# Performance work log

Hardware: AMD Instinct MI355X
Metric: run time of the kernel (lower is better)

Reference implementation:

```python
import jax, jax.numpy as jnp
import numpy as np

HEADS = 8
NEG_SLOPE = 0.2


def _layer_norm(x, g, b, eps=1e-5):
    mu = x.mean(-1, keepdims=True)
    var = ((x - mu) ** 2).mean(-1, keepdims=True)
    return (x - mu) / jnp.sqrt(var + eps) * g + b


def setup_inputs() -> dict:
    key = jax.random.key(0)
    ks = jax.random.split(key, 24)
    N, E, H, L = 512, 260000, 256, 4
    s = 0.05
    return dict(
        x=jax.random.normal(ks[0], (N, 1), jnp.float32),
        edge_index=jax.random.randint(ks[1], (2, E), 0, N),
        edge_attr=jax.random.uniform(ks[2], (E, 3), jnp.float32),
        emb_W=jax.random.normal(ks[3], (1, H)) * s,
        emb_b=jnp.zeros((H,)),
        Wl=jax.random.normal(ks[4], (L, H, H)) * s,
        bl=jnp.zeros((L, H)),
        Wr=jax.random.normal(ks[5], (L, H, H)) * s,
        br=jnp.zeros((L, H)),
        We=jax.random.normal(ks[6], (L, 3, H)) * s,
        att=jax.random.normal(ks[7], (L, HEADS, H // HEADS)) * s,
        gb=jnp.zeros((L, H)),
        ln_g=jnp.ones((L, H)),
        ln_b=jnp.zeros((L, H)),
        p1_W=jax.random.normal(ks[8], (2 * H, H)) * s,
        p1_b=jnp.zeros((H,)),
        p2_W=jax.random.normal(ks[9], (H, H // 2)) * s,
        p2_b=jnp.zeros((H // 2,)),
        p3_W=jax.random.normal(ks[10], (H // 2, 1)) * s,
        p3_b=jnp.zeros((1,)),
        v1_W=jax.random.normal(ks[11], (2 * H, H)) * s,
        v1_b=jnp.zeros((H,)),
        v2_W=jax.random.normal(ks[12], (H, 1)) * s,
        v2_b=jnp.zeros((1,)),
        coupling=jnp.asarray(1.0, jnp.float32),
    )


def reference(x, edge_index, edge_attr, emb_W, emb_b, Wl, bl, Wr, br, We, att,
              gb, ln_g, ln_b, p1_W, p1_b, p2_W, p2_b, p3_W, p3_b,
              v1_W, v1_b, v2_W, v2_b, coupling):
    N = x.shape[0]
    E = edge_attr.shape[0]
    L = Wl.shape[0]
    C = Wl.shape[-1] // HEADS
    src, dst = edge_index[0], edge_index[1]

    # PyG GATv2Conv adds self-loops with edge_attr fill_value='mean'
    # (mean of incoming edge_attr per destination node).
    sums = jax.ops.segment_sum(edge_attr, dst, num_segments=N)
    cnt = jax.ops.segment_sum(jnp.ones((E,), edge_attr.dtype), dst, num_segments=N)
    self_attr = sums / jnp.maximum(cnt, 1.0)[:, None]
    loop = jnp.arange(N)
    src_f = jnp.concatenate([src, loop])            # [E+N]
    dst_f = jnp.concatenate([dst, loop])
    ea_f = jnp.concatenate([edge_attr, self_attr])  # [E+N, 3]

    h = x @ emb_W + emb_b                           # [N, H]
    for l in range(L):
        res = h
        xl = (h @ Wl[l] + bl[l]).reshape(N, HEADS, C)
        xr = (h @ Wr[l] + br[l]).reshape(N, HEADS, C)
        ee = (ea_f @ We[l]).reshape(-1, HEADS, C)
        # GATv2 scoring: leaky_relu(x_l[src]+x_r[dst]+edge) . att
        m = jax.nn.leaky_relu(xl[src_f] + xr[dst_f] + ee, NEG_SLOPE)
        alpha = jnp.einsum('ehc,hc->eh', m, att[l])
        amax = jax.ops.segment_max(alpha, dst_f, num_segments=N)
        alpha = jnp.exp(alpha - amax[dst_f])
        denom = jax.ops.segment_sum(alpha, dst_f, num_segments=N)
        alpha = alpha / denom[dst_f]
        out = jax.ops.segment_sum(xl[src_f] * alpha[..., None], dst_f,
                                  num_segments=N).reshape(N, HEADS * C) + gb[l]
        h = jax.nn.relu(_layer_norm(out + res, ln_g[l], ln_b[l]))

    # graph-level representation (single graph, batch=None branch)
    graph_repr = jnp.concatenate([h.mean(0, keepdims=True),
                                  h.max(0, keepdims=True)], axis=1)  # [1, 2H]

    # all-pairs edge representations (i < j)
    iu, ju = jnp.triu_indices(N, k=1)
    er = jnp.concatenate([h[iu], h[ju]], axis=1)    # [N(N-1)/2, 2H]
    p = jax.nn.relu(er @ p1_W + p1_b)
    p = jax.nn.relu(p @ p2_W + p2_b)
    policy_logits = (p @ p3_W + p3_b).squeeze(-1)   # [N(N-1)/2]

    v = jax.nn.relu(graph_repr @ v1_W + v1_b)
    value = (v @ v2_W + v2_b).squeeze(-1)           # [1]

    # Potts energy: per-color degree-squared approximation of triangles
    colors = jnp.argmax(edge_attr, axis=1)
    energy = jnp.asarray(0.0, h.dtype)
    for c in (1, 2):
        w = (colors == c).astype(h.dtype)
        deg = (jax.ops.segment_sum(w, src, num_segments=N)
               + jax.ops.segment_sum(w, dst, num_segments=N))
        energy = energy + (deg ** 2).sum() / (2.0 * N)
    energy = energy * coupling

    return policy_logits, value, energy
```

## Files before the change

### kernel.cpp

```cpp
#include <hip/hip_runtime.h>
#include <math.h>

#define HDIM 256
#define NHEADS 8
#define NEG 0.2f
#define NB 256
#define SEG 4

typedef float f32x4 __attribute__((ext_vector_type(4)));
typedef _Float16 f16x8 __attribute__((ext_vector_type(8)));
typedef __fp16 fp16v2 __attribute__((ext_vector_type(2)));

__global__ __launch_bounds__(256) void edge_part(
    const int* __restrict__ ei, const float* __restrict__ ea, int E, int CH,
    int* __restrict__ pcnt, float* __restrict__ psum, int* __restrict__ pcol) {
  __shared__ int   lcnt[512];
  __shared__ float ls0[512], ls1[512], ls2[512];
  __shared__ int   lcol[1024];
  int t = threadIdx.x, b = blockIdx.x;
  for (int n = t; n < 512; n += 256) {
    lcnt[n] = 0; ls0[n] = 0.f; ls1[n] = 0.f; ls2[n] = 0.f;
    lcol[n] = 0; lcol[512 + n] = 0;
  }
  __syncthreads();
  int e0 = b * CH, e1 = min(E, e0 + CH);
  for (int e = e0 + t; e < e1; e += 256) {
    int src = ei[e], dst = ei[E + e];
    float a0 = ea[3*e], a1 = ea[3*e+1], a2 = ea[3*e+2];
    atomicAdd(&lcnt[dst], 1);
    atomicAdd(&ls0[dst], a0);
    atomicAdd(&ls1[dst], a1);
    atomicAdd(&ls2[dst], a2);
    int idx = 0; float best = a0;
    if (a1 > best) { best = a1; idx = 1; }
    if (a2 > best) { idx = 2; }
    if (idx) {
      int o = (idx - 1) << 9;
      atomicAdd(&lcol[o + src], 1);
      atomicAdd(&lcol[o + dst], 1);
    }
  }
  __syncthreads();
  for (int n = t; n < 512; n += 256) {
    pcnt[b*512 + n] = lcnt[n];
    psum[(size_t)(0*NB + b)*512 + n] = ls0[n];
    psum[(size_t)(1*NB + b)*512 + n] = ls1[n];
    psum[(size_t)(2*NB + b)*512 + n] = ls2[n];
    pcol[(size_t)(0*NB + b)*512 + n] = lcol[n];
    pcol[(size_t)(1*NB + b)*512 + n] = lcol[512 + n];
  }
}

__global__ __launch_bounds__(256) void red_kernel(
    const int* __restrict__ pcnt, const float* __restrict__ psum,
    const int* __restrict__ pcol,
    int* __restrict__ cnt, float* __restrict__ sred, int* __restrict__ dred,
    int* __restrict__ pbase) {
  int q = blockIdx.x >> 1;
  int n = (blockIdx.x & 1)*256 + threadIdx.x;
  if (q == 0) {
    int run = 0;
#pragma unroll 8
    for (int b = 0; b < NB; ++b) {
      int v = pcnt[b*512 + n];
      pbase[b*512 + n] = run;
      run += v;
    }
    cnt[n] = run;
  } else if (q <= 3) {
    int qq = q - 1;
    float s = 0.f;
#pragma unroll 8
    for (int b = 0; b < NB; ++b) s += psum[(size_t)(qq*NB + b)*512 + n];
    sred[qq*512 + n] = s;
  } else {
    int qq = q - 4;
    int s = 0;
#pragma unroll 8
    for (int b = 0; b < NB; ++b) s += pcol[(size_t)(qq*NB + b)*512 + n];
    dred[qq*512 + n] = s;
  }
}

__global__ __launch_bounds__(512) void scan2(
    const int* __restrict__ cnt, const float* __restrict__ sred,
    const int* __restrict__ dred, int N,
    int* __restrict__ rowp, float4* __restrict__ csr,
    const float* __restrict__ coupling, float* __restrict__ eout) {
  int t = threadIdx.x;
  int c = (t < N) ? cnt[t] : 0;
  __shared__ int sbuf[512];
  int v = (t < N) ? (c + 1) : 0;
  sbuf[t] = v;
  __syncthreads();
  for (int off = 1; off < 512; off <<= 1) {
    int add = (t >= off) ? sbuf[t - off] : 0;
    __syncthreads();
    sbuf[t] += add;
    __syncthreads();
  }
  int incl = sbuf[t], excl = incl - v;
  if (t < N) {
    rowp[t] = excl;
    if (t == N - 1) rowp[N] = incl;
    float inv = 1.f / fmaxf((float)c, 1.f);
    csr[excl] = make_float4(sred[t]*inv, sred[512 + t]*inv, sred[1024 + t]*inv,
                            __int_as_float(t));
  }
  float e = 0.f;
  if (t < N) {
    float d1 = (float)dred[t], d2 = (float)dred[512 + t];
    e = d1*d1 + d2*d2;
  }
#pragma unroll
  for (int off = 1; off < 64; off <<= 1) e += __shfl_xor(e, off);
  __shared__ float wred[8];
  if ((t & 63) == 0) wred[t >> 6] = e;
  __syncthreads();
  if (t == 0) {
    float s = 0.f;
#pragma unroll
    for (int i = 0; i < 8; ++i) s += wred[i];
    eout[0] = coupling[0] * s / (2.f * (float)N);
  }
}

__global__ __launch_bounds__(256) void scatter2(
    const int* __restrict__ ei, const float* __restrict__ ea, int E, int CH,
    const int* __restrict__ rowp, const int* __restrict__ pbase,
    float4* __restrict__ csr) {
  __shared__ int lofs[512];
  int t = threadIdx.x, b = blockIdx.x;
  for (int n = t; n < 512; n += 256) lofs[n] = 0;
  __syncthreads();
  int e0 = b * CH, e1 = min(E, e0 + CH);
  for (int e = e0 + t; e < e1; e += 256) {
    int src = ei[e], dst = ei[E + e];
    float a0 = ea[3*e], a1 = ea[3*e+1], a2 = ea[3*e+2];
    int lp = atomicAdd(&lofs[dst], 1);
    int pos = rowp[dst] + 1 + pbase[b*512 + dst] + lp;
    csr[pos] = make_float4(a0, a1, a2, __int_as_float(src));
  }
}

__global__ __launch_bounds__(256) void emb_kernel(
    const float* __restrict__ x, const float* __restrict__ eW,
    const float* __restrict__ eb, float* __restrict__ h) {
  int n = blockIdx.x, t = threadIdx.x;
  h[n*HDIM + t] = fmaf(x[n], eW[t], eb[t]);
}

__global__ __launch_bounds__(256) void w_prep_all(
    const float* __restrict__ Wl, const float* __restrict__ Wr,
    const float* __restrict__ p1W, unsigned short* __restrict__ dst) {
  int gid = blockIdx.x * 256 + threadIdx.x;
  int s = gid >> 16, e = gid & 65535;
  int k = e >> 8, n = e & 255;
  const float* src = (s < 4) ? (Wl + (size_t)s*65536)
                   : (s < 8) ? (Wr + (size_t)(s-4)*65536)
                             : (p1W + (size_t)(s-8)*65536);
  int c = k >> 5, quad = (k >> 3) & 3, kj = k & 7;
  int nt = n >> 4, nl = n & 15;
  int lane = quad*16 + nl;
  _Float16 hv = (_Float16)src[(size_t)k*256 + n];
  dst[(size_t)s*65536 + ((nt*8 + c)*512 + lane*8 + kj)] = *(unsigned short*)&hv;
}

__global__ __launch_bounds__(256) void dual_gemm_mfma(
    const float* __restrict__ Hm,
    const unsigned short* __restrict__ W1h, const unsigned short* __restrict__ W2h,
    const float* __restrict__ b1, const float* __restrict__ b2,
    float* __restrict__ o1, float* __restrict__ o2,
    unsigned short* __restrict__ o1h) {
  int bx = blockIdx.x, by = blockIdx.y;
  int t = threadIdx.x, w = t >> 6, l = t & 63;
  int quad = l >> 4, nl = l & 15;
  int mt = bx*4 + w;

  const unsigned short* Wh; const float* bias; float* o; int nt;
  bool first = (by < 16);
  if (first) { Wh = W1h; bias = b1; o = o1; nt = by; }
  else       { Wh = W2h; bias = b2; o = o2; nt = by - 16; }

  const float* Ar = Hm + (size_t)(mt*16 + nl)*HDIM + quad*8;
  f32x4 acc = (f32x4){0.f, 0.f, 0.f, 0.f};

#pragma unroll
  for (int c = 0; c < 8; ++c) {
    float4 a0 = *(const float4*)(Ar + c*32);
    float4 a1 = *(const float4*)(Ar + c*32 + 4);
    union { f16x8 v8; fp16v2 v2[4]; } u;
    u.v2[0] = __builtin_amdgcn_cvt_pkrtz(a0.x, a0.y);
    u.v2[1] = __builtin_amdgcn_cvt_pkrtz(a0.z, a0.w);
    u.v2[2] = __builtin_amdgcn_cvt_pkrtz(a1.x, a1.y);
    u.v2[3] = __builtin_amdgcn_cvt_pkrtz(a1.z, a1.w);
    f16x8 bfrag = *(const f16x8*)(Wh + (size_t)((nt*8 + c)*512 + l*8));
    acc = __builtin_amdgcn_mfma_f32_16x16x32_f16(u.v8, bfrag, acc, 0, 0, 0);
  }

  int colg = nt*16 + nl;
  float bv = bias ? bias[colg] : 0.f;
#pragma unroll
  for (int r = 0; r < 4; ++r) {
    float val = acc[r] + bv;
    size_t idx = (size_t)(mt*16 + quad*4 + r)*HDIM + colg;
    o[idx] = val;
    if (first && o1h) {
      _Float16 hv = (_Float16)val;
      o1h[idx] = *(unsigned short*)&hv;
    }
  }
}

__global__ __launch_bounds__(256) void attn_gather(
    const unsigned short* __restrict__ xlh, const float* __restrict__ xr,
    const float4* __restrict__ csr, const int* __restrict__ row_start,
    const float* __restrict__ We, const float* __restrict__ att,
    float* __restrict__ pm, float* __restrict__ pl, float* __restrict__ pacc) {
  int nb = blockIdx.x;
  int n = nb >> 2, sgm = nb & (SEG - 1);
  int t = threadIdx.x;
  int g = t >> 5, l = t & 31, hd = l >> 2, qd = l & 3;
  int cb = hd*32 + qd*8;

  float xrv[8], w0[8], w1[8], w2[8], av[8];
#pragma unroll
  for (int j = 0; j < 8; ++j) {
    xrv[j] = xr[(size_t)n*HDIM + cb + j];
    w0[j]  = We[cb + j];
    w1[j]  = We[HDIM + cb + j];
    w2[j]  = We[2*HDIM + cb + j];
    av[j]  = att[cb + j];
  }
  int rs = row_start[n], re = row_start[n+1], len = re - rs;
  int s0 = rs + ((len * sgm) >> 2);
  int s1 = rs + ((len * (sgm + 1)) >> 2);

  float mh = -INFINITY, lh = 0.f;
  float acc[8] = {0.f,0.f,0.f,0.f,0.f,0.f,0.f,0.f};

  int idx = s0 + g;
  if (idx < s1) {
    float4 rec = csr[idx];
    while (idx < s1) {
      int idxn = idx + 8;
      float4 recn = csr[idxn < s1 ? idxn : rs];
      int s = __float_as_int(rec.w);
      union { f16x8 v8; _Float16 h[8]; } ux;
      ux.v8 = *(const f16x8*)(xlh + (size_t)s*HDIM + cb);
      float xv[8];
#pragma unroll
      for (int j = 0; j < 8; ++j) xv[j] = (float)ux.h[j];
      float partial = 0.f;
#pragma unroll
      for (int j = 0; j < 8; ++j) {
        float m = fmaf(rec.z, w2[j], fmaf(rec.y, w1[j], fmaf(rec.x, w0[j], xrv[j]))) + xv[j];
        m = fmaxf(m, NEG * m);
        partial = fmaf(m, av[j], partial);
      }
      partial += __shfl_xor(partial, 1);
      partial += __shfl_xor(partial, 2);
      if (partial > mh) {
        float sc = __expf(mh - partial);
        lh *= sc;
#pragma unroll
        for (int j = 0; j < 8; ++j) acc[j] *= sc;
        mh = partial;
      }
      float pw = __expf(partial - mh);
      lh += pw;
#pragma unroll
      for (int j = 0; j < 8; ++j) acc[j] = fmaf(pw, xv[j], acc[j]);
      rec = recn; idx = idxn;
    }
  }

  __shared__ float lacc[8][HDIM];
  __shared__ float lm[8][NHEADS];
  __shared__ float llv[8][NHEADS];
#pragma unroll
  for (int j = 0; j < 8; ++j) lacc[g][cb + j] = acc[j];
  if (qd == 0) { lm[g][hd] = mh; llv[g][hd] = lh; }
  __syncthreads();

  int c = t, hh = c >> 5;
  float M = -INFINITY;
#pragma unroll
  for (int g2 = 0; g2 < 8; ++g2) M = fmaxf(M, lm[g2][hh]);
  float L = 0.f, o = 0.f;
#pragma unroll
  for (int g2 = 0; g2 < 8; ++g2) {
    float e2 = __expf(lm[g2][hh] - M);
    L = fmaf(llv[g2][hh], e2, L);
    o = fmaf(lacc[g2][c], e2, o);
  }
  pacc[(size_t)nb*HDIM + c] = o;
  if ((c & 31) == 0) {
    pm[nb*NHEADS + hh] = M;
    pl[nb*NHEADS + hh] = L;
  }
}

__global__ __launch_bounds__(256) void attn_merge(
    const float* __restrict__ pm, const float* __restrict__ pl,
    const float* __restrict__ pacc,
    const float* __restrict__ gb, const float* __restrict__ lng,
    const float* __restrict__ lnb,
    const float* __restrict__ h_in, float* __restrict__ h_out) {
  int n = blockIdx.x, t = threadIdx.x;
  int c = t, hh = c >> 5;
  float M = -INFINITY;
#pragma unroll
  for (int s = 0; s < SEG; ++s) M = fmaxf(M, pm[(n*SEG + s)*NHEADS + hh]);
  float L = 0.f, o = 0.f;
#pragma unroll
  for (int s = 0; s < SEG; ++s) {
    float e2 = __expf(pm[(n*SEG + s)*NHEADS + hh] - M);
    L = fmaf(pl[(n*SEG + s)*NHEADS + hh], e2, L);
    o = fmaf(pacc[(size_t)(n*SEG + s)*HDIM + c], e2, o);
  }
  float val = o / L + gb[c] + h_in[(size_t)n*HDIM + c];

  float s1 = val, s2 = val * val;
#pragma unroll
  for (int off = 1; off < 64; off <<= 1) {
    s1 += __shfl_xor(s1, off);
    s2 += __shfl_xor(s2, off);
  }
  __shared__ float rs1[4], rs2[4];
  if ((t & 63) == 0) { rs1[t >> 6] = s1; rs2[t >> 6] = s2; }
  __syncthreads();
  float S1 = rs1[0] + rs1[1] + rs1[2] + rs1[3];
  float S2 = rs2[0] + rs2[1] + rs2[2] + rs2[3];
  float mu = S1 * (1.f/HDIM);
  float var = S2 * (1.f/HDIM) - mu * mu;
  float y = (val - mu) * rsqrtf(var + 1e-5f);
  y = fmaf(y, lng[c], lnb[c]);
  h_out[(size_t)n*HDIM + c] = fmaxf(y, 0.f);
}

__global__ __launch_bounds__(256) void w2_prep_kernel(
    const float* __restrict__ W2, unsigned short* __restrict__ W2h) {
  int tid = blockIdx.x * 256 + threadIdx.x;
  int k = tid >> 7, n = tid & 127;
  int c = k >> 5, kq = (k >> 3) & 3, kj = k & 7;
  int nt = n >> 4, nl = n & 15;
  int lane = kq*16 + nl;
  _Float16 hv = (_Float16)W2[(size_t)k*128 + n];
  W2h[(size_t)(((c*8 + nt)*64 + lane)*8 + kj)] = *(unsigned short*)&hv;
}

__global__ __launch_bounds__(256, 4) void pair_mfma_kernel(
    const float* __restrict__ A, const float* __restrict__ Bm,
    const unsigned short* __restrict__ W2h,
    const float* __restrict__ b2, const float* __restrict__ W3,
    const float* __restrict__ b3, float* __restrict__ out, int N) {
  int bb = blockIdx.x;
  int half = bb & 1;
  int b = bb >> 1, ti = 0, rem = 32;
  while (b >= rem) { b -= rem; ti++; rem--; }
  int tj = ti + b;
  int i0 = ti * 16 + half * 8;
  int j0 = tj * 16;

  int t = threadIdx.x;
  int w = t >> 6, l = t & 63;
  int quad = l >> 4, nl = l & 15;

  float b2v[8], w3v[8];
#pragma unroll
  for (int nt = 0; nt < 8; ++nt) {
    b2v[nt] = b2[nt*16 + nl];
    w3v[nt] = W3[nt*16 + nl];
  }

  const float* Brow = Bm + (size_t)(j0 + nl) * HDIM;
  const float* Arow0 = A + (size_t)(i0 + w*2) * HDIM;

  f32x4 acc[2][8];
#pragma unroll
  for (int a2 = 0; a2 < 2; ++a2)
#pragma unroll
    for (int nt = 0; nt < 8; ++nt) acc[a2][nt] = (f32x4){0.f,0.f,0.f,0.f};

  for (int c = 0; c < 8; ++c) {
    int kb = c*32 + quad*8;
    float4 bv0 = *(const float4*)(Brow + kb);
    float4 bv1 = *(const float4*)(Brow + kb + 4);

    f16x8 afrag[2];
#pragma unroll
    for (int a2 = 0; a2 < 2; ++a2) {
      const float* Ar = Arow0 + (size_t)a2*HDIM + kb;
      float4 av0 = *(const float4*)Ar;
      float4 av1 = *(const float4*)(Ar + 4);
      union { f16x8 v8; fp16v2 v2[4]; } u;
      u.v2[0] = __builtin_amdgcn_cvt_pkrtz(fmaxf(av0.x + bv0.x, 0.f),
                                           fmaxf(av0.y + bv0.y, 0.f));
      u.v2[1] = __builtin_amdgcn_cvt_pkrtz(fmaxf(av0.z + bv0.z, 0.f),
                                           fmaxf(av0.w + bv0.w, 0.f));
      u.v2[2] = __builtin_amdgcn_cvt_pkrtz(fmaxf(av1.x + bv1.x, 0.f),
                                           fmaxf(av1.y + bv1.y, 0.f));
      u.v2[3] = __builtin_amdgcn_cvt_pkrtz(fmaxf(av1.z + bv1.z, 0.f),
                                           fmaxf(av1.w + bv1.w, 0.f));
      afrag[a2] = u.v8;
    }

#pragma unroll
    for (int nt = 0; nt < 8; ++nt) {
      f16x8 bfrag = *(const f16x8*)(W2h + (size_t)(((c*8 + nt)*64 + l) * 8));
#pragma unroll
      for (int a2 = 0; a2 < 2; ++a2)
        acc[a2][nt] = __builtin_amdgcn_mfma_f32_16x16x32_f16(
            afrag[a2], bfrag, acc[a2][nt], 0, 0, 0);
    }
  }

  float b3v = b3[0];
#pragma unroll
  for (int a2 = 0; a2 < 2; ++a2) {
    int i = i0 + w*2 + a2;
#pragma unroll
    for (int r = 0; r < 4; ++r) {
      float s = 0.f;
#pragma unroll
      for (int nt = 0; nt < 8; ++nt)
        s = fmaf(fmaxf(acc[a2][nt][r] + b2v[nt], 0.f), w3v[nt], s);
      s += __shfl_xor(s, 1);
      s += __shfl_xor(s, 2);
      s += __shfl_xor(s, 4);
      s += __shfl_xor(s, 8);
      if (nl == 0) {
        int j = j0 + quad*4 + r;
        if (i < j)
          out[(size_t)i*(2*N - i - 1)/2 + (j - i - 1)] = s + b3v;
      }
    }
  }
}

__global__ __launch_bounds__(256) void pool_kernel(
    const float* __restrict__ h, float* __restrict__ psums,
    float* __restrict__ pmaxs) {
  int g = blockIdx.x, t = threadIdx.x;
  float s = 0.f, m = -INFINITY;
#pragma unroll
  for (int r = 0; r < 16; ++r) {
    float v = h[(size_t)(g*16 + r)*HDIM + t];
    s += v; m = fmaxf(m, v);
  }
  psums[g*HDIM + t] = s;
  pmaxs[g*HDIM + t] = m;
}

__global__ __launch_bounds__(256) void value1_kernel(
    const float* __restrict__ psums, const float* __restrict__ pmaxs,
    const float* __restrict__ v1W, float* __restrict__ vpart, int N) {
  int b = blockIdx.x, t = threadIdx.x;
  int k0 = b * 16;
  int kk = t >> 4, g = t & 15;
  __shared__ float repr16[16];
  int k = k0 + kk;
  float v;
  if (k < HDIM) {
    v = psums[g*HDIM + k] + psums[(g + 16)*HDIM + k];
    v += __shfl_xor(v, 1); v += __shfl_xor(v, 2);
    v += __shfl_xor(v, 4); v += __shfl_xor(v, 8);
    if (g == 0) repr16[kk] = v / (float)N;
  } else {
    int kc = k - HDIM;
    v = fmaxf(pmaxs[g*HDIM + kc], pmaxs[(g + 16)*HDIM + kc]);
    v = fmaxf(v, __shfl_xor(v, 1)); v = fmaxf(v, __shfl_xor(v, 2));
    v = fmaxf(v, __shfl_xor(v, 4)); v = fmaxf(v, __shfl_xor(v, 8));
    if (g == 0) repr16[kk] = v;
  }
  __syncthreads();
  float pv = 0.f;
#pragma unroll
  for (int q = 0; q < 16; ++q)
    pv = fmaf(repr16[q], v1W[(size_t)(k0 + q)*HDIM + t], pv);
  vpart[b*HDIM + t] = pv;
}

__global__ __launch_bounds__(256) void value2_kernel(
    const float* __restrict__ vpart, const float* __restrict__ v1b,
    const float* __restrict__ v2W, const float* __restrict__ v2b,
    float* __restrict__ out) {
  int t = threadIdx.x;
  float a = 0.f;
#pragma unroll
  for (int g = 0; g < 32; ++g) a += vpart[g*HDIM + t];
  a = fmaxf(a + v1b[t], 0.f);
  float pv = a * v2W[t];
#pragma unroll
  for (int off = 1; off < 64; off <<= 1) pv += __shfl_xor(pv, off);
  __shared__ float wsum[4];
  if ((t & 63) == 0) wsum[t >> 6] = pv;
  __syncthreads();
  if (t == 0) out[0] = wsum[0] + wsum[1] + wsum[2] + wsum[3] + v2b[0];
}

extern "C" void kernel_launch(void* const* d_in, const int* in_sizes, int n_in,
                              void* d_out, int out_size, void* d_ws, size_t ws_size,
                              hipStream_t stream) {
  const float* x    = (const float*)d_in[0];
  const int*   ei   = (const int*)  d_in[1];
  const float* ea   = (const float*)d_in[2];
  const float* embW = (const float*)d_in[3];
  const float* embb = (const float*)d_in[4];
  const float* Wl   = (const float*)d_in[5];
  const float* bl   = (const float*)d_in[6];
  const float* Wr   = (const float*)d_in[7];
  const float* br   = (const float*)d_in[8];
  const float* We   = (const float*)d_in[9];
  const float* att  = (const float*)d_in[10];
  const float* gb   = (const float*)d_in[11];
  const float* lng  = (const float*)d_in[12];
  const float* lnb  = (const float*)d_in[13];
  const float* p1W  = (const float*)d_in[14];
  const float* p1b  = (const float*)d_in[15];
  const float* p2W  = (const float*)d_in[16];
  const float* p2b  = (const float*)d_in[17];
  const float* p3W  = (const float*)d_in[18];
  const float* p3b  = (const float*)d_in[19];
  const float* v1W  = (const float*)d_in[20];
  const float* v1b  = (const float*)d_in[21];
  const float* v2W  = (const float*)d_in[22];
  const float* v2b  = (const float*)d_in[23];
  const float* coup = (const float*)d_in[24];

  int N = in_sizes[0];
  int E = in_sizes[2] / 3;
  float* out = (float*)d_out;
  size_t P = (size_t)N*(N-1)/2;

  char* w = (char*)d_ws;
  int*    rowp = (int*)   (w + 0);
  float*  plS  = (float*) (w + 2560);
  float*  plM  = (float*) (w + 35328);
  float*  vprt = (float*) (w + 68096);
  float4* csr  = (float4*)(w + 101120);
  size_t csr_end = 101120 + (size_t)(E + N) * 16;
  csr_end = (csr_end + 255) & ~(size_t)255;
  float* hA  = (float*)(w + csr_end);
  float* hB  = hA  + (size_t)N*HDIM;
  float* xlb = hB  + (size_t)N*HDIM;
  float* xrb = xlb + (size_t)N*HDIM;
  float* Ab  = xrb + (size_t)N*HDIM;
  float* Bb  = Ab  + (size_t)N*HDIM;
  unsigned short* xlh   = (unsigned short*)(Bb + (size_t)N*HDIM);
  unsigned short* W2h   = xlh + (size_t)N*HDIM;
  unsigned short* Whall = W2h + 32768;
  size_t ubase = ((size_t)((char*)(Whall + 10*65536) - w) + 255) & ~(size_t)255;

  char* U = w + ubase;
  int*    pcnt = (int*)   (U + 0);
  float*  psum = (float*) (U + 524288);
  int*    pcol = (int*)   (U + 2097152);
  int*    pbase= (int*)   (U + 3145728);
  int*    cnt  = (int*)   (U + 3670016);
  float*  sred = (float*) (U + 3672064);
  int*    dred = (int*)   (U + 3678208);
  float*  pmv  = (float*) (U + 0);
  float*  plv  = (float*) (U + 65536);
  float*  pacc = (float*) (U + 131072);

  int CH = (E + NB - 1) / NB;
  edge_part<<<NB, 256, 0, stream>>>(ei, ea, E, CH, pcnt, psum, pcol);
  red_kernel<<<12, 256, 0, stream>>>(pcnt, psum, pcol, cnt, sred, dred, pbase);
  scan2<<<1, 512, 0, stream>>>(cnt, sred, dred, N, rowp, csr, coup, out + P + 1);
  scatter2<<<NB, 256, 0, stream>>>(ei, ea, E, CH, rowp, pbase, csr);
  emb_kernel<<<N, 256, 0, stream>>>(x, embW, embb, hA);
  w2_prep_kernel<<<128, 256, 0, stream>>>(p2W, W2h);
  w_prep_all<<<2560, 256, 0, stream>>>(Wl, Wr, p1W, Whall);

  float* hin = hA;
  float* hout = hB;
  for (int l = 0; l < 4; ++l) {
    dual_gemm_mfma<<<dim3(8, 32), 256, 0, stream>>>(hin,
        Whall + (size_t)l*65536, Whall + (size_t)(4 + l)*65536,
        bl + l*HDIM, br + l*HDIM, xlb, xrb, xlh);
    attn_gather<<<N*SEG, 256, 0, stream>>>(xlh, xrb, csr, rowp,
        We + (size_t)l*3*HDIM, att + (size_t)l*HDIM, pmv, plv, pacc);
    attn_merge<<<N, 256, 0, stream>>>(pmv, plv, pacc,
        gb + (size_t)l*HDIM, lng + (size_t)l*HDIM, lnb + (size_t)l*HDIM,
        hin, hout);
    float* tmp = hin; hin = hout; hout = tmp;
  }

  dual_gemm_mfma<<<dim3(8, 32), 256, 0, stream>>>(hin,
      Whall + (size_t)8*65536, Whall + (size_t)9*65536,
      p1b, (const float*)nullptr, Ab, Bb, (unsigned short*)nullptr);

  pair_mfma_kernel<<<1056, 256, 0, stream>>>(Ab, Bb, W2h, p2b, p3W, p3b, out, N);

  pool_kernel<<<32, 256, 0, stream>>>(hin, plS, plM);
  value1_kernel<<<32, 256, 0, stream>>>(plS, plM, v1W, vprt, N);
  value2_kernel<<<1, 256, 0, stream>>>(vprt, v1b, v2W, v2b, out + P);
}
```

Measured before the change: 315.1 us.

## Fuse embedding into first layer kernels, merge weight prep, prefetch gather rows

Removes the standalone embedding kernel: when no hidden input is given, the first dual GEMM and the first attention merge recompute x*embW+embb on the fly. The W2 fp16 repack joins the main weight-prep launch, which cuts two kernel launches in total. The attention gather loop also software-pipelines one more step, loading the next source row's fp16 features while computing the current edge to hide gather latency. The trade-off is extra branching and a few more registers in the hot kernels.

```diff
diff --git a/kernel.cpp b/kernel.cpp
--- a/kernel.cpp
+++ b/kernel.cpp
@@ -143,31 +143,37 @@
   }
 }
 
-__global__ __launch_bounds__(256) void emb_kernel(
-    const float* __restrict__ x, const float* __restrict__ eW,
-    const float* __restrict__ eb, float* __restrict__ h) {
-  int n = blockIdx.x, t = threadIdx.x;
-  h[n*HDIM + t] = fmaf(x[n], eW[t], eb[t]);
-}
-
 __global__ __launch_bounds__(256) void w_prep_all(
     const float* __restrict__ Wl, const float* __restrict__ Wr,
-    const float* __restrict__ p1W, unsigned short* __restrict__ dst) {
+    const float* __restrict__ p1W, const float* __restrict__ W2,
+    unsigned short* __restrict__ dst, unsigned short* __restrict__ W2h) {
   int gid = blockIdx.x * 256 + threadIdx.x;
-  int s = gid >> 16, e = gid & 65535;
-  int k = e >> 8, n = e & 255;
-  const float* src = (s < 4) ? (Wl + (size_t)s*65536)
-                   : (s < 8) ? (Wr + (size_t)(s-4)*65536)
-                             : (p1W + (size_t)(s-8)*65536);
-  int c = k >> 5, quad = (k >> 3) & 3, kj = k & 7;
-  int nt = n >> 4, nl = n & 15;
-  int lane = quad*16 + nl;
-  _Float16 hv = (_Float16)src[(size_t)k*256 + n];
-  dst[(size_t)s*65536 + ((nt*8 + c)*512 + lane*8 + kj)] = *(unsigned short*)&hv;
+  if (gid < 10*65536) {
+    int s = gid >> 16, e = gid & 65535;
+    int k = e >> 8, n = e & 255;
+    const float* src = (s < 4) ? (Wl + (size_t)s*65536)
+                     : (s < 8) ? (Wr + (size_t)(s-4)*65536)
+                               : (p1W + (size_t)(s-8)*65536);
+    int c = k >> 5, quad = (k >> 3) & 3, kj = k & 7;
+    int nt = n >> 4, nl = n & 15;
+    int lane = quad*16 + nl;
+    _Float16 hv = (_Float16)src[(size_t)k*256 + n];
+    dst[(size_t)s*65536 + ((nt*8 + c)*512 + lane*8 + kj)] = *(unsigned short*)&hv;
+  } else {
+    int e = gid - 10*65536;
+    int k = e >> 7, n = e & 127;
+    int c = k >> 5, kq = (k >> 3) & 3, kj = k & 7;
+    int nt = n >> 4, nl = n & 15;
+    int lane = kq*16 + nl;
+    _Float16 hv = (_Float16)W2[(size_t)k*128 + n];
+    W2h[(size_t)(((c*8 + nt)*64 + lane)*8 + kj)] = *(unsigned short*)&hv;
+  }
 }
 
 __global__ __launch_bounds__(256) void dual_gemm_mfma(
     const float* __restrict__ Hm,
+    const float* __restrict__ x, const float* __restrict__ embW,
+    const float* __restrict__ embb,
     const unsigned short* __restrict__ W1h, const unsigned short* __restrict__ W2h,
     const float* __restrict__ b1, const float* __restrict__ b2,
     float* __restrict__ o1, float* __restrict__ o2,
@@ -182,13 +188,28 @@
   if (first) { Wh = W1h; bias = b1; o = o1; nt = by; }
   else       { Wh = W2h; bias = b2; o = o2; nt = by - 16; }
 
-  const float* Ar = Hm + (size_t)(mt*16 + nl)*HDIM + quad*8;
+  int row = mt*16 + nl;
+  const float* Ar = Hm ? (Hm + (size_t)row*HDIM + quad*8) : nullptr;
+  float xm = Hm ? 0.f : x[row];
   f32x4 acc = (f32x4){0.f, 0.f, 0.f, 0.f};
 
 #pragma unroll
   for (int c = 0; c < 8; ++c) {
-    float4 a0 = *(const float4*)(Ar + c*32);
-    float4 a1 = *(const float4*)(Ar + c*32 + 4);
+    float4 a0, a1;
+    if (Hm) {
+      a0 = *(const float4*)(Ar + c*32);
+      a1 = *(const float4*)(Ar + c*32 + 4);
+    } else {
+      int kb = c*32 + quad*8;
+      float4 e0 = *(const float4*)(embW + kb);
+      float4 e1 = *(const float4*)(embW + kb + 4);
+      float4 c0 = *(const float4*)(embb + kb);
+      float4 c1 = *(const float4*)(embb + kb + 4);
+      a0 = make_float4(fmaf(xm, e0.x, c0.x), fmaf(xm, e0.y, c0.y),
+                       fmaf(xm, e0.z, c0.z), fmaf(xm, e0.w, c0.w));
+      a1 = make_float4(fmaf(xm, e1.x, c1.x), fmaf(xm, e1.y, c1.y),
+                       fmaf(xm, e1.z, c1.z), fmaf(xm, e1.w, c1.w));
+    }
     union { f16x8 v8; fp16v2 v2[4]; } u;
     u.v2[0] = __builtin_amdgcn_cvt_pkrtz(a0.x, a0.y);
     u.v2[1] = __builtin_amdgcn_cvt_pkrtz(a0.z, a0.w);
@@ -242,15 +263,18 @@
   int idx = s0 + g;
   if (idx < s1) {
     float4 rec = csr[idx];
+    int idx1 = idx + 8;
+    float4 rec1 = csr[idx1 < s1 ? idx1 : rs];
+    union { f16x8 v8; _Float16 h[8]; } cur, nxt;
+    cur.v8 = *(const f16x8*)(xlh + (size_t)__float_as_int(rec.w)*HDIM + cb);
     while (idx < s1) {
-      int idxn = idx + 8;
-      float4 recn = csr[idxn < s1 ? idxn : rs];
-      int s = __float_as_int(rec.w);
-      union { f16x8 v8; _Float16 h[8]; } ux;
-      ux.v8 = *(const f16x8*)(xlh + (size_t)s*HDIM + cb);
+      int idx2 = idx1 + 8;
+      float4 rec2 = csr[idx2 < s1 ? idx2 : rs];
+      nxt.v8 = *(const f16x8*)(xlh +
+                (size_t)__float_as_int(rec1.w)*HDIM + cb);
       float xv[8];
 #pragma unroll
-      for (int j = 0; j < 8; ++j) xv[j] = (float)ux.h[j];
+      for (int j = 0; j < 8; ++j) xv[j] = (float)cur.h[j];
       float partial = 0.f;
 #pragma unroll
       for (int j = 0; j < 8; ++j) {
@@ -271,7 +295,8 @@
       lh += pw;
 #pragma unroll
       for (int j = 0; j < 8; ++j) acc[j] = fmaf(pw, xv[j], acc[j]);
-      rec = recn; idx = idxn;
+      rec = rec1; rec1 = rec2; cur.v8 = nxt.v8;
+      idx = idx1; idx1 = idx2;
     }
   }
 
@@ -306,7 +331,10 @@
     const float* __restrict__ pacc,
     const float* __restrict__ gb, const float* __restrict__ lng,
     const float* __restrict__ lnb,
-    const float* __restrict__ h_in, float* __restrict__ h_out) {
+    const float* __restrict__ h_in,
+    const float* __restrict__ x, const float* __restrict__ embW,
+    const float* __restrict__ embb,
+    float* __restrict__ h_out) {
   int n = blockIdx.x, t = threadIdx.x;
   int c = t, hh = c >> 5;
   float M = -INFINITY;
@@ -319,7 +347,8 @@
     L = fmaf(pl[(n*SEG + s)*NHEADS + hh], e2, L);
     o = fmaf(pacc[(size_t)(n*SEG + s)*HDIM + c], e2, o);
   }
-  float val = o / L + gb[c] + h_in[(size_t)n*HDIM + c];
+  float hi = h_in ? h_in[(size_t)n*HDIM + c] : fmaf(x[n], embW[c], embb[c]);
+  float val = o / L + gb[c] + hi;
 
   float s1 = val, s2 = val * val;
 #pragma unroll
@@ -337,17 +366,6 @@
   float y = (val - mu) * rsqrtf(var + 1e-5f);
   y = fmaf(y, lng[c], lnb[c]);
   h_out[(size_t)n*HDIM + c] = fmaxf(y, 0.f);
-}
-
-__global__ __launch_bounds__(256) void w2_prep_kernel(
-    const float* __restrict__ W2, unsigned short* __restrict__ W2h) {
-  int tid = blockIdx.x * 256 + threadIdx.x;
-  int k = tid >> 7, n = tid & 127;
-  int c = k >> 5, kq = (k >> 3) & 3, kj = k & 7;
-  int nt = n >> 4, nl = n & 15;
-  int lane = kq*16 + nl;
-  _Float16 hv = (_Float16)W2[(size_t)k*128 + n];
-  W2h[(size_t)(((c*8 + nt)*64 + lane)*8 + kj)] = *(unsigned short*)&hv;
 }
 
 __global__ __launch_bounds__(256, 4) void pair_mfma_kernel(
@@ -570,25 +588,24 @@
   red_kernel<<<12, 256, 0, stream>>>(pcnt, psum, pcol, cnt, sred, dred, pbase);
   scan2<<<1, 512, 0, stream>>>(cnt, sred, dred, N, rowp, csr, coup, out + P + 1);
   scatter2<<<NB, 256, 0, stream>>>(ei, ea, E, CH, rowp, pbase, csr);
-  emb_kernel<<<N, 256, 0, stream>>>(x, embW, embb, hA);
-  w2_prep_kernel<<<128, 256, 0, stream>>>(p2W, W2h);
-  w_prep_all<<<2560, 256, 0, stream>>>(Wl, Wr, p1W, Whall);
-
-  float* hin = hA;
+  w_prep_all<<<2688, 256, 0, stream>>>(Wl, Wr, p1W, p2W, Whall, W2h);
+
+  float* hin = nullptr;
   float* hout = hB;
   for (int l = 0; l < 4; ++l) {
-    dual_gemm_mfma<<<dim3(8, 32), 256, 0, stream>>>(hin,
+    dual_gemm_mfma<<<dim3(8, 32), 256, 0, stream>>>(hin, x, embW, embb,
         Whall + (size_t)l*65536, Whall + (size_t)(4 + l)*65536,
         bl + l*HDIM, br + l*HDIM, xlb, xrb, xlh);
     attn_gather<<<N*SEG, 256, 0, stream>>>(xlh, xrb, csr, rowp,
         We + (size_t)l*3*HDIM, att + (size_t)l*HDIM, pmv, plv, pacc);
     attn_merge<<<N, 256, 0, stream>>>(pmv, plv, pacc,
         gb + (size_t)l*HDIM, lng + (size_t)l*HDIM, lnb + (size_t)l*HDIM,
-        hin, hout);
-    float* tmp = hin; hin = hout; hout = tmp;
-  }
-
-  dual_gemm_mfma<<<dim3(8, 32), 256, 0, stream>>>(hin,
+        hin, x, embW, embb, hout);
+    hin = hout;
+    hout = (hout == hB) ? hA : hB;
+  }
+
+  dual_gemm_mfma<<<dim3(8, 32), 256, 0, stream>>>(hin, x, embW, embb,
       Whall + (size_t)8*65536, Whall + (size_t)9*65536,
       p1b, (const float*)nullptr, Ab, Bb, (unsigned short*)nullptr);
 
```

New measurement: 309.9 us. About the same (-1.6%).
